# Optimization experiments

Hardware: AMD Instinct MI355X
Metric: run time of the kernel (lower is better)

Reference implementation:

```python
import jax, jax.numpy as jnp
import numpy as np

WIN_LEN = 48  # int(1.6 * fps) with fps = 30.0


def setup_inputs() -> dict:
    key = jax.random.key(0)
    k1, k2 = jax.random.split(key)
    B, N, C = 1, 400000, 3
    # RGB means of face-skin pixels: positive values; shift uniform away from 0
    rgbs = jax.random.uniform(k1, (B, N, C), dtype=jnp.float32) + 0.25
    # Projection matrix fixed to POS matrix M, as in the module's __init__
    W = jnp.array([[0.0, 1.0, -1.0], [-2.0, 1.0, 1.0]], dtype=jnp.float32)
    # nn.Linear bias is left at its (random) init; it cancels in the math but keep it faithful
    b = jax.random.normal(k2, (2,), dtype=jnp.float32) * 0.02
    return {"rgbs": rgbs, "W": W, "b": b}


def reference(rgbs, W, b):
    B, N, C = rgbs.shape  # B must be 1 for the overlap-add path (as in the torch code)
    win = WIN_LEN
    K = N - win  # torch loop is range(0, N - win_len): the last window is dropped
    x = rgbs[0]  # [N, 3]

    # sliding windows via gather: idx[k, w] = k + w
    idx = jnp.arange(K, dtype=jnp.int32)[:, None] + jnp.arange(win, dtype=jnp.int32)[None, :]
    wins = x[idx]

    # temporal normalization per window
    Cn = wins / jnp.mean(wins, axis=1, keepdims=True)

    # linear projection 3 -> 2 (POS plane)
    S = jnp.einsum('kwc,oc->kwo', Cn, W) + b

    # std over the window dim, unbiased (torch default ddof=1)
    std = jnp.std(S, axis=1, ddof=1)  # [K, 2]
    h = S[..., 0] + (std[:, 0] / std[:, 1])[:, None] * S[..., 1]
    h = h - jnp.mean(h, axis=1, keepdims=True)
    h = jax.lax.stop_gradient(h)  # torch: h = h.detach()

    H = jnp.zeros((N,), dtype=rgbs.dtype).at[idx].add(h)
    return H[None, :]  # [1, N]
```

## Files before the change

### kernel.cpp

```cpp
#include <hip/hip_runtime.h>
#include <math.h>

#define WIN  48
#define HALO 47
#define BLK  256
#define TH   5
#define TA   7
#define RR   (BLK * TH)
#define RA   (RR + HALO)
#define XR   (RR + 2 * HALO)

__global__ __launch_bounds__(BLK) void pos_fused_kernel(
    const float* __restrict__ x,
    const float* __restrict__ Wm,
    float* __restrict__ H, int N, int K)
{
    __shared__ float xs[3][XR + 3];
    __shared__ float as[3][RA + TA];

    const int t     = threadIdx.x;
    const int n0    = blockIdx.x * RR;
    const int xbase = n0 - HALO;

    for (int i = t; i < XR * 3; i += BLK) {
        int row = i / 3;
        int c   = i - row * 3;
        int g   = xbase + row;
        g = g < 0 ? 0 : (g > N - 1 ? N - 1 : g);
        xs[c][row] = x[g * 3 + c];
    }
    __syncthreads();

    const float W00 = Wm[0], W01 = Wm[1], W02 = Wm[2];
    const float W10 = Wm[3], W11 = Wm[4], W12 = Wm[5];
    const float c000 = W00*W00, c011 = W01*W01, c022 = W02*W02;
    const float c001 = 2.f*W00*W01, c002 = 2.f*W00*W02, c012 = 2.f*W01*W02;
    const float c100 = W10*W10, c111 = W11*W11, c122 = W12*W12;
    const float c101 = 2.f*W10*W11, c102 = 2.f*W10*W12, c112 = 2.f*W11*W12;

    const int abase = t * TA;
    if (abase < RA) {
        float s0=0.f,s1=0.f,s2=0.f;
        float S00=0.f,S01=0.f,S02=0.f,S11=0.f,S12=0.f,S22=0.f;
        float st0[TA-1], st1[TA-1], st2[TA-1];
        #pragma unroll
        for (int w = 0; w < WIN; ++w) {
            float x0 = xs[0][abase+w], x1 = xs[1][abase+w], x2 = xs[2][abase+w];
            if (w < TA-1) { st0[w]=x0; st1[w]=x1; st2[w]=x2; }
            s0+=x0; s1+=x1; s2+=x2;
            S00=fmaf(x0,x0,S00); S01=fmaf(x0,x1,S01); S02=fmaf(x0,x2,S02);
            S11=fmaf(x1,x1,S11); S12=fmaf(x1,x2,S12); S22=fmaf(x2,x2,S22);
        }
        #pragma unroll
        for (int j = 0; j < TA; ++j) {
            if (j > 0) {
                float xn0=xs[0][abase+HALO+j], xn1=xs[1][abase+HALO+j], xn2=xs[2][abase+HALO+j];
                float xo0=st0[j-1], xo1=st1[j-1], xo2=st2[j-1];
                s0 += xn0-xo0; s1 += xn1-xo1; s2 += xn2-xo2;
                S00 += fmaf(xn0,xn0,-xo0*xo0); S01 += fmaf(xn0,xn1,-xo0*xo1);
                S02 += fmaf(xn0,xn2,-xo0*xo2); S11 += fmaf(xn1,xn1,-xo1*xo1);
                S12 += fmaf(xn1,xn2,-xo1*xo2); S22 += fmaf(xn2,xn2,-xo2*xo2);
            }
            float y0 = 48.f/s0, y1 = 48.f/s1, y2 = 48.f/s2;
            float p00 = y0*y0*S00, p11 = y1*y1*S11, p22 = y2*y2*S22;
            float p01 = y0*y1*S01, p02 = y0*y2*S02, p12 = y1*y2*S12;
            float q0 = c000*p00 + c011*p11 + c022*p22 + c001*p01 + c002*p02 + c012*p12;
            float q1 = c100*p00 + c111*p11 + c122*p22 + c101*p01 + c102*p02 + c112*p12;
            float r  = sqrtf(q0 / q1);
            int  k   = xbase + abase + j;
            bool ok  = (k >= 0) & (k < K);
            as[0][abase+j] = ok ? (W00 + r*W10)*y0 : 0.f;
            as[1][abase+j] = ok ? (W01 + r*W11)*y1 : 0.f;
            as[2][abase+j] = ok ? (W02 + r*W12)*y2 : 0.f;
        }
    }
    __syncthreads();

    const int hbase = t * TH;
    float A0=0.f, A1=0.f, A2=0.f;
    float sa0[TH-1], sa1[TH-1], sa2[TH-1];
    #pragma unroll
    for (int w = 0; w < WIN; ++w) {
        float a0 = as[0][hbase+w], a1 = as[1][hbase+w], a2 = as[2][hbase+w];
        if (w < TH-1) { sa0[w]=a0; sa1[w]=a1; sa2[w]=a2; }
        A0+=a0; A1+=a1; A2+=a2;
    }
    #pragma unroll
    for (int j = 0; j < TH; ++j) {
        if (j > 0) {
            A0 += as[0][hbase+HALO+j] - sa0[j-1];
            A1 += as[1][hbase+HALO+j] - sa1[j-1];
            A2 += as[2][hbase+HALO+j] - sa2[j-1];
        }
        int xrow = hbase + j + HALO;
        float h = xs[0][xrow]*A0 + xs[1][xrow]*A1 + xs[2][xrow]*A2;
        int n = n0 + hbase + j;
        if (n < N) H[n] = h;
    }
}

extern "C" void kernel_launch(void* const* d_in, const int* in_sizes, int n_in,
                              void* d_out, int out_size, void* d_ws, size_t ws_size,
                              hipStream_t stream) {
    const float* rgbs = (const float*)d_in[0];
    const float* W    = (const float*)d_in[1];

    const int N = in_sizes[0] / 3;
    const int K = N - WIN;
    float* H = (float*)d_out;

    const int blocks = (N + RR - 1) / RR;
    pos_fused_kernel<<<blocks, BLK, 0, stream>>>(rgbs, W, H, N, K);
}
```

Measured before the change: 65.46 us.

## Vectorize interior tile loads with float4 and enlarge per-thread output tiles

Interior blocks now load the RGB tile with aligned float4 reads and de-interleave them into per-channel shared arrays, with scalar prologue and epilogue handling for misalignment. Edge blocks keep the clamped scalar path. The per-thread output and coefficient tile sizes grow from 5/7 to 7/9, so each block covers more samples and the halo recompute is amortized over more outputs. In exchange there are fewer blocks (about 224 for this N), which may underfill the GPU's compute units, plus more shared memory and registers per thread.

```diff
diff --git a/kernel.cpp b/kernel.cpp
--- a/kernel.cpp
+++ b/kernel.cpp
@@ -4,30 +4,57 @@
 #define WIN  48
 #define HALO 47
 #define BLK  256
-#define TH   5
-#define TA   7
+#define TH   7
+#define TA   9
 #define RR   (BLK * TH)
 #define RA   (RR + HALO)
 #define XR   (RR + 2 * HALO)
+#define XPAD 16
+#define APAD 8
 
 __global__ __launch_bounds__(BLK) void pos_fused_kernel(
     const float* __restrict__ x,
     const float* __restrict__ Wm,
     float* __restrict__ H, int N, int K)
 {
-    __shared__ float xs[3][XR + 3];
-    __shared__ float as[3][RA + TA];
+    __shared__ float xs[3][XR + XPAD];
+    __shared__ float as[3][RA + APAD];
 
     const int t     = threadIdx.x;
     const int n0    = blockIdx.x * RR;
     const int xbase = n0 - HALO;
 
-    for (int i = t; i < XR * 3; i += BLK) {
-        int row = i / 3;
-        int c   = i - row * 3;
-        int g   = xbase + row;
-        g = g < 0 ? 0 : (g > N - 1 ? N - 1 : g);
-        xs[c][row] = x[g * 3 + c];
+    const bool interior = (xbase >= 0) && (xbase + XR <= N);
+    if (interior) {
+        const int F0  = xbase * 3;
+        const int pre = (4 - (F0 & 3)) & 3;
+        if (t < pre) {
+            int f = F0 + t, r = f / 3, c = f - 3 * r;
+            xs[c][r - xbase] = x[f];
+        }
+        const int n4  = (XR * 3 - pre) >> 2;
+        const int rem = (XR * 3 - pre) & 3;
+        const float4* x4 = (const float4*)(x + F0 + pre);
+        for (int i = t; i < n4; i += BLK) {
+            float4 v = x4[i];
+            int f = F0 + pre + 4 * i;
+            int r = f / 3, c = f - 3 * r; r -= xbase;
+            xs[c][r] = v.x; if (++c == 3) { c = 0; ++r; }
+            xs[c][r] = v.y; if (++c == 3) { c = 0; ++r; }
+            xs[c][r] = v.z; if (++c == 3) { c = 0; ++r; }
+            xs[c][r] = v.w;
+        }
+        if (t < rem) {
+            int f = F0 + pre + 4 * n4 + t, r = f / 3, c = f - 3 * r;
+            xs[c][r - xbase] = x[f];
+        }
+    } else {
+        for (int i = t; i < XR * 3; i += BLK) {
+            int r = i / 3, c = i - 3 * r;
+            int g = xbase + r;
+            g = g < 0 ? 0 : (g > N - 1 ? N - 1 : g);
+            xs[c][r] = x[g * 3 + c];
+        }
     }
     __syncthreads();
 
```

Result: no change. 64.87 us (-0.9%).
